# Performance work log

Measured on AMD Instinct MI355X. Metric: run time of the kernel, lower is better.

The kernel has to match this reference:

```python
import jax, jax.numpy as jnp
import numpy as np

N_EMBD = 1024
NUM_HEADS = 16
HEAD_SIZE = 64


def setup_inputs() -> dict:
    key = jax.random.key(0)
    ks = jax.random.split(key, 6)
    B, T, C, hs = 2, 2048, N_EMBD, HEAD_SIZE
    s = 0.02
    return {
        "x": jax.random.normal(ks[0], (B, T, C), dtype=jnp.float32),
        "Wk": jax.random.normal(ks[1], (hs, C), dtype=jnp.float32) * s,  # torch Linear weight [out,in]
        "Wv": jax.random.normal(ks[2], (hs, C), dtype=jnp.float32) * s,
        "Wq": jax.random.normal(ks[3], (C, C), dtype=jnp.float32) * s,
        "Wp": jax.random.normal(ks[4], (C, C), dtype=jnp.float32) * s,
        "bp": jax.random.normal(ks[5], (C,), dtype=jnp.float32) * s,
    }


def reference(x, Wk, Wv, Wq, Wp, bp):
    B, T, C = x.shape
    H, hs = NUM_HEADS, HEAD_SIZE
    k = x @ Wk.T                      # [B,T,hs]
    v = x @ Wv.T                      # [B,T,hs]
    q = x @ Wq.T                      # [B,T,C]
    # Faithful to torch: raw view of [B,T,C] -> [B,H,T,hs] (row-major reshape, not transpose)
    q = q.reshape(B, H, T, hs)
    k = k.reshape(B, 1, T, hs)
    v = v.reshape(B, 1, T, hs)
    att = jnp.einsum("bhqd,bhkd->bhqk", q, jnp.broadcast_to(k, (B, 1, T, hs))) * (hs ** -0.5)
    mask = jnp.tril(jnp.ones((T, T), dtype=bool))[None, None]  # [1,1,T,T]
    att = jnp.where(mask, att, -jnp.inf)
    att = jax.nn.softmax(att, axis=-1)
    y = jnp.einsum("bhqk,bhkd->bhqd", att, jnp.broadcast_to(v, (B, 1, T, hs)))  # [B,H,T,hs]
    y = jnp.transpose(y, (0, 2, 1, 3)).reshape(B, T, C)
    return y @ Wp.T + bp
```

## Files before the change

kernel.cpp:

```cpp
#include <hip/hip_runtime.h>
#include <cstddef>
#include <cstdint>

#define B_N 2
#define T_N 2048
#define C_N 1024
#define H_N 16
#define HS_N 64
#define M_N (B_N * T_N)

typedef __attribute__((ext_vector_type(8))) short bf16x8;
typedef __attribute__((ext_vector_type(4))) float f32x4;
typedef __attribute__((ext_vector_type(4))) unsigned int u32x4;
typedef __attribute__((ext_vector_type(2))) unsigned int u32x2;

#define QSCALE 0.18033688011112042f

__device__ __forceinline__ ushort f2bf(float f) {
    union { float f; uint32_t u; } v; v.f = f;
    uint32_t r = v.u + 0x7fffu + ((v.u >> 16) & 1u);
    return (ushort)(r >> 16);
}
__device__ __forceinline__ unsigned pack2_trunc(float a, float b) {
    union { float f; uint32_t u; } x, y; x.f = a; y.f = b;
    return (x.u >> 16) | (y.u & 0xFFFF0000u);
}

#define GLL16(g, l)                                                         \
    __builtin_amdgcn_global_load_lds(                                       \
        (const __attribute__((address_space(1))) unsigned int*)(g),         \
        (__attribute__((address_space(3))) unsigned int*)(l), 16, 0, 0)

__global__ void cvt_all_kernel(const float* __restrict__ x,
                               const float* __restrict__ Wq,
                               const float* __restrict__ Wp,
                               const float* __restrict__ Wk,
                               const float* __restrict__ Wv,
                               ushort* __restrict__ xb,
                               ushort* __restrict__ Wqb,
                               ushort* __restrict__ Wpb,
                               ushort* __restrict__ Wkvb) {
    const int S0 = M_N * C_N / 4;
    const int S1 = S0 + C_N * C_N / 4;
    const int S2 = S1 + C_N * C_N / 4;
    const int S3 = S2 + HS_N * C_N / 4;
    const int S4 = S3 + HS_N * C_N / 4;
    const int stride = gridDim.x * blockDim.x;
    for (int i = blockIdx.x * blockDim.x + threadIdx.x; i < S4; i += stride) {
        const float* src; ushort* dst; int j; float sc = 1.f;
        if (i < S0)      { src = x;  dst = xb;   j = i; }
        else if (i < S1) { src = Wq; dst = Wqb;  j = i - S0; sc = QSCALE; }
        else if (i < S2) { src = Wp; dst = Wpb;  j = i - S1; }
        else if (i < S3) { src = Wk; dst = Wkvb; j = i - S2; }
        else             { src = Wv; dst = Wkvb + HS_N * C_N; j = i - S3; }
        const float4 f = ((const float4*)src)[j];
        ushort4 o;
        o.x = f2bf(f.x * sc); o.y = f2bf(f.y * sc);
        o.z = f2bf(f.z * sc); o.w = f2bf(f.w * sc);
        ((ushort4*)dst)[j] = o;
    }
}

template <int MODE>
__global__ __launch_bounds__(256, 2) void gemm_bf16(
    const ushort* __restrict__ A,
    const ushort* __restrict__ W,
    const float* __restrict__ bias,
    void* __restrict__ Cout,
    ushort* __restrict__ kb,
    ushort* __restrict__ vbt,
    int K)
{
    __shared__ __align__(16) ushort As[64 * 64];
    __shared__ __align__(16) ushort Bs[128 * 64];
    const int flat = blockIdx.x + (blockIdx.y << 6);
    const int m0 = (((flat & 7) << 3) | ((flat >> 3) & 7)) * 64;
    const int n0 = (flat >> 6) * 128;
    const int tid = threadIdx.x;
    const int wid = tid >> 6;
    const int lane = tid & 63;
    const int ln = lane & 15;
    const int quad = lane >> 4;
    const int wm = wid >> 1, wn = wid & 1;

    f32x4 acc[2][4];
    #pragma unroll
    for (int i = 0; i < 2; ++i)
        #pragma unroll
        for (int j = 0; j < 4; ++j)
            acc[i][j] = (f32x4){0.f, 0.f, 0.f, 0.f};

    const int srow = lane >> 3;
    const int schk = (lane & 7) ^ srow;

    for (int k0 = 0; k0 < K; k0 += 64) {
        __syncthreads();
        #pragma unroll
        for (int t = 0; t < 2; ++t) {
            const int seg = wid * 2 + t;
            GLL16(A + (size_t)(m0 + seg * 8 + srow) * K + k0 + schk * 8,
                  As + seg * 512);
        }
        #pragma unroll
        for (int t = 0; t < 4; ++t) {
            const int seg = wid * 4 + t;
            GLL16(W + (size_t)(n0 + seg * 8 + srow) * K + k0 + schk * 8,
                  Bs + seg * 512);
        }
        __syncthreads();

        #pragma unroll
        for (int hh = 0; hh < 2; ++hh) {
            bf16x8 af[2], bf[4];
            const int sw = ln & 7;
            #pragma unroll
            for (int i = 0; i < 2; ++i) {
                const int row = wm * 32 + i * 16 + ln;
                af[i] = *(const bf16x8*)&As[row * 64 + (((hh * 4 + quad) ^ sw) * 8)];
            }
            #pragma unroll
            for (int j = 0; j < 4; ++j) {
                const int row = wn * 64 + j * 16 + ln;
                bf[j] = *(const bf16x8*)&Bs[row * 64 + (((hh * 4 + quad) ^ sw) * 8)];
            }
            #pragma unroll
            for (int i = 0; i < 2; ++i)
                #pragma unroll
                for (int j = 0; j < 4; ++j)
                    acc[i][j] = __builtin_amdgcn_mfma_f32_16x16x32_bf16(
                        af[i], bf[j], acc[i][j], 0, 0, 0);
        }
    }

    if (MODE == 1 && n0 >= C_N) {
        #pragma unroll
        for (int i = 0; i < 2; ++i) {
            const int row0 = m0 + wm * 32 + i * 16 + quad * 4;
            #pragma unroll
            for (int j = 0; j < 4; ++j) {
                const int c2 = wn * 64 + j * 16 + ln;
                if (c2 >= 64) {
                    const int d = c2 - 64;
                    const int b = row0 >> 11;
                    const int t0 = row0 & 2047;
                    ushort4 pk;
                    pk.x = f2bf(acc[i][j][0]); pk.y = f2bf(acc[i][j][1]);
                    pk.z = f2bf(acc[i][j][2]); pk.w = f2bf(acc[i][j][3]);
                    *(ushort4*)&vbt[((size_t)b * 64 + d) * T_N + t0] = pk;
                } else {
                    #pragma unroll
                    for (int reg = 0; reg < 4; ++reg)
                        kb[(size_t)(row0 + reg) * 64 + c2] = f2bf(acc[i][j][reg]);
                }
            }
        }
        return;
    }

    #pragma unroll
    for (int i = 0; i < 2; ++i) {
        #pragma unroll
        for (int j = 0; j < 4; ++j) {
            const int col = n0 + wn * 64 + j * 16 + ln;
            const float bv = (MODE == 0) ? bias[col] : 0.f;
            #pragma unroll
            for (int reg = 0; reg < 4; ++reg) {
                const int row = m0 + wm * 32 + i * 16 + quad * 4 + reg;
                const float v = acc[i][j][reg] + bv;
                if (MODE == 0)
                    ((float*)Cout)[(size_t)row * C_N + col] = v;
                else
                    ((ushort*)Cout)[(size_t)row * C_N + col] = f2bf(v);
            }
        }
    }
}

__global__ __launch_bounds__(256, 2) void attn_mfma_kernel(
    const ushort* __restrict__ qb,
    const ushort* __restrict__ kb,
    const ushort* __restrict__ vbt,
    ushort* __restrict__ yb)
{
    __shared__ __align__(16) ushort smem[32768];

    const int bh = blockIdx.x;
    const int b = bh >> 4, h = bh & 15;
    const int yy = blockIdx.y;
    const int qt = (yy < 8) ? 31 - yy : (yy < 16) ? yy - 8
                 : (yy < 24) ? 39 - yy : yy - 16;
    const int nkt = (qt >> 1) + 1;
    const int qmax = qt * 64 + 63;

    const int tid = threadIdx.x;
    const int w = tid >> 6;
    const int lane = tid & 63;
    const int ln = lane & 15;
    const int quad = lane >> 4;

    const ushort* kbase = kb + (size_t)b * T_N * HS_N;
    const ushort* vtbase = vbt + (size_t)b * HS_N * T_N;

    bf16x8 qf[4][2];
    {
        const ushort* qs_ = qb + (size_t)b * T_N * C_N
                          + (size_t)h * T_N * HS_N
                          + (size_t)(qt * 64) * HS_N;
        #pragma unroll
        for (int q4 = 0; q4 < 4; ++q4)
            #pragma unroll
            for (int kc = 0; kc < 2; ++kc)
                qf[q4][kc] = *(const bf16x8*)(qs_ + (q4 * 16 + ln) * HS_N
                                              + kc * 32 + quad * 8);
    }

    auto stage = [&](int buf, int k0) {
        ushort* Ksb = smem + buf * 16384;
        ushort* Vtb = Ksb + 8192;
        #pragma unroll
        for (int i = 0; i < 4; ++i) {
            const int x = (i * 4 + w) * 64 + lane;
            const int key = x >> 3, slk = x & 7;
            GLL16(kbase + (size_t)(k0 + key) * HS_N + ((slk ^ (key & 7)) * 8),
                  Ksb + (i * 4 + w) * 512);
            const int d = x >> 4, slv = x & 15;
            GLL16(vtbase + (size_t)d * T_N + k0 + ((slv ^ (d & 15)) * 8),
                  Vtb + (i * 4 + w) * 512);
        }
    };

    f32x4 o[4][4];
    #pragma unroll
    for (int i = 0; i < 4; ++i)
        #pragma unroll
        for (int j = 0; j < 4; ++j)
            o[i][j] = (f32x4){0.f, 0.f, 0.f, 0.f};
    float lac[4] = {0.f, 0.f, 0.f, 0.f};

    stage(0, 0);

    for (int kt = 0; kt < nkt; ++kt) {
        __syncthreads();
        if (kt + 1 < nkt) stage((kt + 1) & 1, (kt + 1) * 128);

        const int k0 = kt * 128;
        const bool dg = (kt == nkt - 1);
        const int kw0 = k0 + w * 32;
        if (dg && kw0 > qmax) continue;

        const ushort* Ksb = smem + (kt & 1) * 16384;
        const ushort* Vtb = Ksb + 8192;

        bf16x8 kf[2][2], vf[4];
        #pragma unroll
        for (int nt = 0; nt < 2; ++nt)
            #pragma unroll
            for (int kc = 0; kc < 2; ++kc) {
                const int key = w * 32 + nt * 16 + ln;
                kf[nt][kc] = *(const bf16x8*)
                    &Ksb[key * 64 + (((kc * 4 + quad) ^ (key & 7)) * 8)];
            }
        #pragma unroll
        for (int db = 0; db < 4; ++db) {
            const int d = db * 16 + ln;
            vf[db] = *(const bf16x8*)
                &Vtb[d * 128 + (((w * 4 + quad) ^ (d & 15)) * 8)];
        }

        f32x4 sc[2][4];
        #pragma unroll
        for (int nt = 0; nt < 2; ++nt)
            #pragma unroll
            for (int q4 = 0; q4 < 4; ++q4) {
                f32x4 s = (f32x4){0.f, 0.f, 0.f, 0.f};
                s = __builtin_amdgcn_mfma_f32_16x16x32_bf16(kf[nt][0], qf[q4][0], s, 0, 0, 0);
                s = __builtin_amdgcn_mfma_f32_16x16x32_bf16(kf[nt][1], qf[q4][1], s, 0, 0, 0);
                sc[nt][q4] = s;
            }

        unsigned pk[2][4][2];
        #pragma unroll
        for (int nt = 0; nt < 2; ++nt)
            #pragma unroll
            for (int q4 = 0; q4 < 4; ++q4) {
                f32x4 s = sc[nt][q4];
                if (dg) {
                    const int qg = qt * 64 + q4 * 16 + ln;
                    #pragma unroll
                    for (int reg = 0; reg < 4; ++reg) {
                        const int key = kw0 + nt * 16 + quad * 4 + reg;
                        if (key > qg) s[reg] = -1e30f;
                    }
                }
                const float p0 = __builtin_amdgcn_exp2f(s[0]);
                const float p1 = __builtin_amdgcn_exp2f(s[1]);
                const float p2 = __builtin_amdgcn_exp2f(s[2]);
                const float p3 = __builtin_amdgcn_exp2f(s[3]);
                lac[q4] += (p0 + p1) + (p2 + p3);
                pk[nt][q4][0] = pack2_trunc(p0, p1);
                pk[nt][q4][1] = pack2_trunc(p2, p3);
            }

        #pragma unroll
        for (int q4 = 0; q4 < 4; ++q4) {
            u32x2 ab0 = __builtin_amdgcn_permlane32_swap(pk[0][q4][0], pk[1][q4][0], false, false);
            u32x2 rs0 = __builtin_amdgcn_permlane16_swap(ab0[0], ab0[1], false, false);
            u32x2 ab1 = __builtin_amdgcn_permlane32_swap(pk[0][q4][1], pk[1][q4][1], false, false);
            u32x2 rs1 = __builtin_amdgcn_permlane16_swap(ab1[0], ab1[1], false, false);
            u32x4 pw;
            pw[0] = rs0[0]; pw[1] = rs1[0]; pw[2] = rs0[1]; pw[3] = rs1[1];
            const bf16x8 pf = __builtin_bit_cast(bf16x8, pw);
            #pragma unroll
            for (int db = 0; db < 4; ++db)
                o[db][q4] = __builtin_amdgcn_mfma_f32_16x16x32_bf16(
                    vf[db], pf, o[db][q4], 0, 0, 0);
        }
    }

    #pragma unroll
    for (int q4 = 0; q4 < 4; ++q4) {
        lac[q4] += __shfl_xor(lac[q4], 16);
        lac[q4] += __shfl_xor(lac[q4], 32);
    }

    float* Ored = (float*)smem;
    const int qloc = 16 * w + (lane >> 2);
    float inv = 0.f;

    #pragma unroll
    for (int pass = 0; pass < 2; ++pass) {
        __syncthreads();
        #pragma unroll
        for (int db2 = 0; db2 < 2; ++db2)
            #pragma unroll
            for (int q4 = 0; q4 < 4; ++q4)
                *(f32x4*)&Ored[(w * 64 + q4 * 16 + ln) * 36 + db2 * 16 + quad * 4]
                    = o[pass * 2 + db2][q4];
        if (pass == 0 && quad == 0) {
            #pragma unroll
            for (int q4 = 0; q4 < 4; ++q4)
                Ored[(w * 64 + q4 * 16 + ln) * 36 + 32] = lac[q4];
        }
        __syncthreads();

        f32x4 a0 = (f32x4){0.f, 0.f, 0.f, 0.f};
        f32x4 a1 = (f32x4){0.f, 0.f, 0.f, 0.f};
        float ls = 0.f;
        #pragma unroll
        for (int v = 0; v < 4; ++v) {
            const int base = (v * 64 + qloc) * 36;
            a0 += *(const f32x4*)&Ored[base + (lane & 3) * 4];
            a1 += *(const f32x4*)&Ored[base + 16 + (lane & 3) * 4];
            if (pass == 0) ls += Ored[base + 32];
        }
        if (pass == 0) inv = 1.0f / ls;

        const int qg = qt * 64 + qloc;
        ushort* yrow = yb + ((size_t)b * T_N + qg) * C_N + h * HS_N
                       + pass * 32 + (lane & 3) * 4;
        ushort4 s0, s1;
        s0.x = f2bf(a0[0] * inv); s0.y = f2bf(a0[1] * inv);
        s0.z = f2bf(a0[2] * inv); s0.w = f2bf(a0[3] * inv);
        s1.x = f2bf(a1[0] * inv); s1.y = f2bf(a1[1] * inv);
        s1.z = f2bf(a1[2] * inv); s1.w = f2bf(a1[3] * inv);
        *(ushort4*)yrow = s0;
        *(ushort4*)(yrow + 16) = s1;
    }
}

extern "C" void kernel_launch(void* const* d_in, const int* in_sizes, int n_in,
                              void* d_out, int out_size, void* d_ws, size_t ws_size,
                              hipStream_t stream) {
    const float* x  = (const float*)d_in[0];
    const float* Wk = (const float*)d_in[1];
    const float* Wv = (const float*)d_in[2];
    const float* Wq = (const float*)d_in[3];
    const float* Wp = (const float*)d_in[4];
    const float* bp = (const float*)d_in[5];
    float* out = (float*)d_out;

    ushort* xb   = (ushort*)d_ws;
    ushort* qb   = xb   + (size_t)M_N * C_N;
    ushort* yb   = qb   + (size_t)M_N * C_N;
    ushort* kbw  = yb   + (size_t)M_N * C_N;
    ushort* vbt  = kbw  + (size_t)M_N * HS_N;
    ushort* Wqb  = vbt  + (size_t)B_N * HS_N * T_N;
    ushort* Wkvb = Wqb  + (size_t)C_N * C_N;
    ushort* Wpb  = Wkvb + (size_t)128 * C_N;

    cvt_all_kernel<<<1024, 256, 0, stream>>>(x, Wq, Wp, Wk, Wv,
                                             xb, Wqb, Wpb, Wkvb);

    gemm_bf16<1><<<dim3(M_N / 64, (C_N + 128) / 128), 256, 0, stream>>>(
        xb, Wqb, nullptr, qb, kbw, vbt, C_N);

    attn_mfma_kernel<<<dim3(B_N * H_N, 32), 256, 0, stream>>>(qb, kbw, vbt, yb);

    gemm_bf16<0><<<dim3(M_N / 64, C_N / 128), 256, 0, stream>>>(
        yb, Wpb, bp, out, nullptr, nullptr, C_N);
}
```

Before: 145.2 us.

## Store K/V in MFMA-fragment order and load directly from global, dropping LDS staging

The projection GEMM epilogue now writes K and V^T in a pre-tiled layout matching the MFMA operand fragments. The attention kernel then reads these fragments with contiguous 16-byte global loads instead of double-buffered LDS staging. This removes the per-tile __syncthreads and the LDS traffic, and shrinks shared memory to the output-reduction buffer, which may raise occupancy. In exchange every wave fetches its K/V fragments from global/L2 with no explicit prefetch, so latency is exposed and blocks of the same head no longer share the data through LDS.

New measurement: 142.5 us. Within noise of the previous version (-1.9%).

```diff
diff --git a/kernel.cpp b/kernel.cpp
--- a/kernel.cpp
+++ b/kernel.cpp
@@ -143,14 +143,21 @@
                     const int d = c2 - 64;
                     const int b = row0 >> 11;
                     const int t0 = row0 & 2047;
+                    const int flatv = ((((t0 >> 5) * 4 + (d >> 4)) * 4
+                                       + ((t0 >> 3) & 3)) * 16 + (d & 15)) * 8
+                                      + (t0 & 7);
                     ushort4 pk;
                     pk.x = f2bf(acc[i][j][0]); pk.y = f2bf(acc[i][j][1]);
                     pk.z = f2bf(acc[i][j][2]); pk.w = f2bf(acc[i][j][3]);
-                    *(ushort4*)&vbt[((size_t)b * 64 + d) * T_N + t0] = pk;
+                    *(ushort4*)&vbt[(size_t)b * HS_N * T_N + flatv] = pk;
                 } else {
                     #pragma unroll
-                    for (int reg = 0; reg < 4; ++reg)
-                        kb[(size_t)(row0 + reg) * 64 + c2] = f2bf(acc[i][j][reg]);
+                    for (int reg = 0; reg < 4; ++reg) {
+                        const int key = row0 + reg;
+                        kb[((((key >> 4) * 2 + (c2 >> 5)) * 4
+                             + ((c2 >> 3) & 3)) * 16 + (key & 15)) * 8
+                           + (c2 & 7)] = f2bf(acc[i][j][reg]);
+                    }
                 }
             }
         }
@@ -182,7 +189,7 @@
     const ushort* __restrict__ vbt,
     ushort* __restrict__ yb)
 {
-    __shared__ __align__(16) ushort smem[32768];
+    __shared__ __align__(16) float Ored[4 * 64 * 36];
 
     const int bh = blockIdx.x;
     const int b = bh >> 4, h = bh & 15;
@@ -198,9 +205,6 @@
     const int ln = lane & 15;
     const int quad = lane >> 4;
 
-    const ushort* kbase = kb + (size_t)b * T_N * HS_N;
-    const ushort* vtbase = vbt + (size_t)b * HS_N * T_N;
-
     bf16x8 qf[4][2];
     {
         const ushort* qs_ = qb + (size_t)b * T_N * C_N
@@ -214,20 +218,7 @@
                                               + kc * 32 + quad * 8);
     }
 
-    auto stage = [&](int buf, int k0) {
-        ushort* Ksb = smem + buf * 16384;
-        ushort* Vtb = Ksb + 8192;
-        #pragma unroll
-        for (int i = 0; i < 4; ++i) {
-            const int x = (i * 4 + w) * 64 + lane;
-            const int key = x >> 3, slk = x & 7;
-            GLL16(kbase + (size_t)(k0 + key) * HS_N + ((slk ^ (key & 7)) * 8),
-                  Ksb + (i * 4 + w) * 512);
-            const int d = x >> 4, slv = x & 15;
-            GLL16(vtbase + (size_t)d * T_N + k0 + ((slv ^ (d & 15)) * 8),
-                  Vtb + (i * 4 + w) * 512);
-        }
-    };
+    const ushort* vbb = vbt + (size_t)b * HS_N * T_N;
 
     f32x4 o[4][4];
     #pragma unroll
@@ -237,35 +228,25 @@
             o[i][j] = (f32x4){0.f, 0.f, 0.f, 0.f};
     float lac[4] = {0.f, 0.f, 0.f, 0.f};
 
-    stage(0, 0);
-
     for (int kt = 0; kt < nkt; ++kt) {
-        __syncthreads();
-        if (kt + 1 < nkt) stage((kt + 1) & 1, (kt + 1) * 128);
-
         const int k0 = kt * 128;
         const bool dg = (kt == nkt - 1);
         const int kw0 = k0 + w * 32;
-        if (dg && kw0 > qmax) continue;
-
-        const ushort* Ksb = smem + (kt & 1) * 16384;
-        const ushort* Vtb = Ksb + 8192;
-
+        if (dg && kw0 > qmax) break;
+
+        const int b16 = ((b * T_N + k0) >> 4) + w * 2;
         bf16x8 kf[2][2], vf[4];
         #pragma unroll
         for (int nt = 0; nt < 2; ++nt)
             #pragma unroll
-            for (int kc = 0; kc < 2; ++kc) {
-                const int key = w * 32 + nt * 16 + ln;
+            for (int kc = 0; kc < 2; ++kc)
                 kf[nt][kc] = *(const bf16x8*)
-                    &Ksb[key * 64 + (((kc * 4 + quad) ^ (key & 7)) * 8)];
-            }
-        #pragma unroll
-        for (int db = 0; db < 4; ++db) {
-            const int d = db * 16 + ln;
+                    &kb[((((b16 + nt) * 2 + kc) * 4 + quad) * 16 + ln) * 8];
+        const int t32 = (k0 >> 5) + w;
+        #pragma unroll
+        for (int db = 0; db < 4; ++db)
             vf[db] = *(const bf16x8*)
-                &Vtb[d * 128 + (((w * 4 + quad) ^ (d & 15)) * 8)];
-        }
+                &vbb[(((t32 * 4 + db) * 4 + quad) * 16 + ln) * 8];
 
         f32x4 sc[2][4];
         #pragma unroll
@@ -323,7 +304,6 @@
         lac[q4] += __shfl_xor(lac[q4], 32);
     }
 
-    float* Ored = (float*)smem;
     const int qloc = 16 * w + (lane >> 2);
     float inv = 0.f;
 
```
